# Optimization experiments

Hardware: AMD Instinct MI355X
Metric: run time of the kernel (lower is better)

Reference implementation:

```python
import jax, jax.numpy as jnp
import numpy as np
from jax import lax

DIM = 256
NUM_HEADS = 8
HEAD_DIM = DIM // NUM_HEADS          # 32
KEY_DIM = int(HEAD_DIM * 0.5)        # 16
SCALE = KEY_DIM ** -0.5
H_QKV = DIM + KEY_DIM * NUM_HEADS * 2  # 512
BN_EPS = 1e-3  # keras BatchNormalization default epsilon


def conv_bn(x, w, gamma, beta, mean, var, groups=1):
    # Conv2D (no bias) + BatchNorm (inference), activation=None
    y = lax.conv_general_dilated(
        x, w, window_strides=(1, 1), padding='SAME',
        dimension_numbers=('NHWC', 'HWIO', 'NHWC'),
        feature_group_count=groups)
    return gamma * (y - mean) * lax.rsqrt(var + BN_EPS) + beta


def setup_inputs() -> dict:
    key = jax.random.key(0)
    ks = jax.random.split(key, 4)
    B, Hs, Ws = 8, 32, 32
    inp = {
        'inputs': jax.random.normal(ks[0], (B, Hs, Ws, DIM), dtype=jnp.float32),
        # qkv: 1x1 conv dim -> h
        'qkv_w': jax.random.normal(ks[1], (1, 1, DIM, H_QKV), dtype=jnp.float32) * 0.05,
        'qkv_gamma': jnp.ones((H_QKV,), jnp.float32),
        'qkv_beta': jnp.zeros((H_QKV,), jnp.float32),
        'qkv_mean': jnp.zeros((H_QKV,), jnp.float32),
        'qkv_var': jnp.ones((H_QKV,), jnp.float32),
        # pe: 3x3 depthwise conv (groups=dim)
        'pe_w': jax.random.normal(ks[2], (3, 3, 1, DIM), dtype=jnp.float32) * 0.05,
        'pe_gamma': jnp.ones((DIM,), jnp.float32),
        'pe_beta': jnp.zeros((DIM,), jnp.float32),
        'pe_mean': jnp.zeros((DIM,), jnp.float32),
        'pe_var': jnp.ones((DIM,), jnp.float32),
        # proj: 1x1 conv dim -> dim
        'proj_w': jax.random.normal(ks[3], (1, 1, DIM, DIM), dtype=jnp.float32) * 0.05,
        'proj_gamma': jnp.ones((DIM,), jnp.float32),
        'proj_beta': jnp.zeros((DIM,), jnp.float32),
        'proj_mean': jnp.zeros((DIM,), jnp.float32),
        'proj_var': jnp.ones((DIM,), jnp.float32),
    }
    return inp


def reference(inputs, qkv_w, qkv_gamma, qkv_beta, qkv_mean, qkv_var,
              pe_w, pe_gamma, pe_beta, pe_mean, pe_var,
              proj_w, proj_gamma, proj_beta, proj_mean, proj_var):
    B, Hs, Ws, C = inputs.shape
    N = Hs * Ws
    x = conv_bn(inputs, qkv_w, qkv_gamma, qkv_beta, qkv_mean, qkv_var)  # [B,H,W,h]
    x = x.reshape(B, N, NUM_HEADS, 2 * KEY_DIM + HEAD_DIM)
    q = x[..., :KEY_DIM]                          # [B,N,nh,kd]
    k = x[..., KEY_DIM:2 * KEY_DIM]               # [B,N,nh,kd]
    v = x[..., 2 * KEY_DIM:]                      # [B,N,nh,hd]
    # attn = q^T @ k^T : [B,nh,N,N]
    attn = jnp.einsum('bnhk,bmhk->bhnm', q, k) * SCALE
    attn = jax.nn.softmax(attn, axis=-1)
    # x = v^T @ attn : [B,nh,hd,N]
    x = jnp.einsum('bnhd,bhnm->bhdm', v, attn)
    # faithful to source: transpose [0,2,1,3] -> [B,hd,nh,N], then reshape NHWC
    x = jnp.transpose(x, (0, 2, 1, 3)).reshape(B, Hs, Ws, C)
    pe = conv_bn(v.reshape(B, Hs, Ws, C), pe_w, pe_gamma, pe_beta, pe_mean, pe_var, groups=C)
    x = x + pe
    x = conv_bn(x, proj_w, proj_gamma, proj_beta, proj_mean, proj_var)
    return x
```

## Files before the change

### kernel.cpp

```cpp
#include <hip/hip_runtime.h>

typedef _Float16 h4 __attribute__((ext_vector_type(4)));
typedef _Float16 h8 __attribute__((ext_vector_type(8)));
typedef float    f4 __attribute__((ext_vector_type(4)));

#define QSCALE (0.25f * 1.44269504088896f)

__device__ __forceinline__ float ex2(float x){ return __builtin_amdgcn_exp2f(x); }

__global__ __launch_bounds__(256) void prep_k(
    const float* __restrict__ qkvw, const float* __restrict__ qg, const float* __restrict__ qb,
    const float* __restrict__ qm,   const float* __restrict__ qv,
    const float* __restrict__ pew,  const float* __restrict__ pg, const float* __restrict__ pb,
    const float* __restrict__ pm,   const float* __restrict__ pv,
    const float* __restrict__ prw,  const float* __restrict__ prg, const float* __restrict__ prb,
    const float* __restrict__ prm,  const float* __restrict__ prv,
    _Float16* __restrict__ Wqkv, float* __restrict__ bqkv,
    _Float16* __restrict__ Wproj, float* __restrict__ bproj,
    float* __restrict__ peW, float* __restrict__ peB)
{
  const int gid = blockIdx.x*256 + threadIdx.x;
  const int gsz = gridDim.x*256;
  for (int i = gid; i < 512*256; i += gsz){
    int o = i >> 8, c = i & 255;
    float s = qg[o] * rsqrtf(qv[o] + 1e-3f);
    Wqkv[i] = (_Float16)(qkvw[c*512 + o] * s);
  }
  for (int i = gid; i < 512; i += gsz){
    float s = qg[i] * rsqrtf(qv[i] + 1e-3f);
    bqkv[i] = qb[i] - qm[i]*s;
  }
  for (int i = gid; i < 256*256; i += gsz){
    int o = i >> 8, c = i & 255;
    float s = prg[o] * rsqrtf(prv[o] + 1e-3f);
    Wproj[i] = (_Float16)(prw[c*256 + o] * s);
  }
  for (int i = gid; i < 256; i += gsz){
    float s = prg[i] * rsqrtf(prv[i] + 1e-3f);
    bproj[i] = prb[i] - prm[i]*s;
  }
  for (int i = gid; i < 9*256; i += gsz){
    int c = i & 255;
    float s = pg[c] * rsqrtf(pv[c] + 1e-3f);
    peW[i] = pew[i] * s;
  }
  for (int i = gid; i < 256; i += gsz){
    float s = pg[i] * rsqrtf(pv[i] + 1e-3f);
    peB[i] = pb[i] - pm[i]*s;
  }
}

__global__ __launch_bounds__(256) void qkv_gemm_k(
    const float* __restrict__ X, const _Float16* __restrict__ Wqkv,
    const float* __restrict__ bias,
    _Float16* __restrict__ Qh, _Float16* __restrict__ Kh, _Float16* __restrict__ Vh)
{
  __shared__ __align__(16) _Float16 As[64*136];
  __shared__ __align__(16) _Float16 Bs[64*136];
  const int t = threadIdx.x, lane = t & 63, wv = t >> 6;
  const int l15 = lane & 15, q = lane >> 4;
  const int wr = wv & 1, wc = wv >> 1;
  const int m0 = blockIdx.x*64, n0 = blockIdx.y*64;
  float4 av[8]; uint4 bv[4];
  #pragma unroll
  for (int i = 0; i < 8; ++i){
    int idx = i*256 + t, row = idx >> 5, c4 = idx & 31;
    av[i] = *(const float4*)(X + (size_t)(m0+row)*256 + c4*4);
  }
  #pragma unroll
  for (int i = 0; i < 4; ++i){
    int idx = i*256 + t, row = idx >> 4, seg = idx & 15;
    bv[i] = *(const uint4*)(Wqkv + (size_t)(n0+row)*256 + seg*8);
  }
  f4 acc[2][2] = {};
  #pragma unroll
  for (int kc = 0; kc < 2; ++kc){
    #pragma unroll
    for (int i = 0; i < 8; ++i){
      int idx = i*256 + t, row = idx >> 5, c4 = idx & 31;
      h4 o; o[0]=(_Float16)av[i].x; o[1]=(_Float16)av[i].y;
            o[2]=(_Float16)av[i].z; o[3]=(_Float16)av[i].w;
      *(h4*)&As[row*136 + c4*4] = o;
    }
    #pragma unroll
    for (int i = 0; i < 4; ++i){
      int idx = i*256 + t, row = idx >> 4, seg = idx & 15;
      *(uint4*)&Bs[row*136 + seg*8] = bv[i];
    }
    __syncthreads();
    if (kc == 0){
      #pragma unroll
      for (int i = 0; i < 8; ++i){
        int idx = i*256 + t, row = idx >> 5, c4 = idx & 31;
        av[i] = *(const float4*)(X + (size_t)(m0+row)*256 + 128 + c4*4);
      }
      #pragma unroll
      for (int i = 0; i < 4; ++i){
        int idx = i*256 + t, row = idx >> 4, seg = idx & 15;
        bv[i] = *(const uint4*)(Wqkv + (size_t)(n0+row)*256 + 128 + seg*8);
      }
    }
    #pragma unroll
    for (int kk = 0; kk < 4; ++kk){
      h8 af[2], bf[2];
      #pragma unroll
      for (int mi = 0; mi < 2; ++mi)
        af[mi] = *(const h8*)&As[(wr*32 + mi*16 + l15)*136 + kk*32 + q*8];
      #pragma unroll
      for (int nj = 0; nj < 2; ++nj)
        bf[nj] = *(const h8*)&Bs[(wc*32 + nj*16 + l15)*136 + kk*32 + q*8];
      #pragma unroll
      for (int mi = 0; mi < 2; ++mi)
      #pragma unroll
      for (int nj = 0; nj < 2; ++nj)
        acc[mi][nj] = __builtin_amdgcn_mfma_f32_16x16x32_f16(af[mi], bf[nj], acc[mi][nj], 0,0,0);
    }
    __syncthreads();
  }
  #pragma unroll
  for (int mi = 0; mi < 2; ++mi)
  #pragma unroll
  for (int nj = 0; nj < 2; ++nj){
    const int og = n0 + wc*32 + nj*16 + l15;
    const int h = og >> 6, j = og & 63;
    const float bs = bias[og];
    #pragma unroll
    for (int r = 0; r < 4; ++r){
      const int mg = m0 + wr*32 + mi*16 + q*4 + r;
      const int b = mg >> 10, n = mg & 1023;
      const size_t bhn = (size_t)(b*8+h)*1024 + n;
      const float v = acc[mi][nj][r] + bs;
      if (j < 16)      Qh[bhn*16 + j]      = (_Float16)(v * QSCALE);
      else if (j < 32) Kh[bhn*16 + (j-16)] = (_Float16)v;
      else             Vh[bhn*32 + (j-32)] = (_Float16)v;
    }
  }
}

__global__ __launch_bounds__(256) void proj_gemm_k(
    const _Float16* __restrict__ A, const _Float16* __restrict__ Wproj,
    const float* __restrict__ bias, float* __restrict__ Out)
{
  __shared__ __align__(16) _Float16 As[64*136];
  __shared__ __align__(16) _Float16 Bs[64*136];
  const int t = threadIdx.x, lane = t & 63, wv = t >> 6;
  const int l15 = lane & 15, q = lane >> 4;
  const int wr = wv & 1, wc = wv >> 1;
  const int m0 = blockIdx.x*64, n0 = blockIdx.y*64;
  uint4 av[4], bv[4];
  #pragma unroll
  for (int i = 0; i < 4; ++i){
    int idx = i*256 + t, row = idx >> 4, seg = idx & 15;
    av[i] = *(const uint4*)(A     + (size_t)(m0+row)*256 + seg*8);
    bv[i] = *(const uint4*)(Wproj + (size_t)(n0+row)*256 + seg*8);
  }
  f4 acc[2][2] = {};
  #pragma unroll
  for (int kc = 0; kc < 2; ++kc){
    #pragma unroll
    for (int i = 0; i < 4; ++i){
      int idx = i*256 + t, row = idx >> 4, seg = idx & 15;
      *(uint4*)&As[row*136 + seg*8] = av[i];
      *(uint4*)&Bs[row*136 + seg*8] = bv[i];
    }
    __syncthreads();
    if (kc == 0){
      #pragma unroll
      for (int i = 0; i < 4; ++i){
        int idx = i*256 + t, row = idx >> 4, seg = idx & 15;
        av[i] = *(const uint4*)(A     + (size_t)(m0+row)*256 + 128 + seg*8);
        bv[i] = *(const uint4*)(Wproj + (size_t)(n0+row)*256 + 128 + seg*8);
      }
    }
    #pragma unroll
    for (int kk = 0; kk < 4; ++kk){
      h8 af[2], bf[2];
      #pragma unroll
      for (int mi = 0; mi < 2; ++mi)
        af[mi] = *(const h8*)&As[(wr*32 + mi*16 + l15)*136 + kk*32 + q*8];
      #pragma unroll
      for (int nj = 0; nj < 2; ++nj)
        bf[nj] = *(const h8*)&Bs[(wc*32 + nj*16 + l15)*136 + kk*32 + q*8];
      #pragma unroll
      for (int mi = 0; mi < 2; ++mi)
      #pragma unroll
      for (int nj = 0; nj < 2; ++nj)
        acc[mi][nj] = __builtin_amdgcn_mfma_f32_16x16x32_f16(af[mi], bf[nj], acc[mi][nj], 0,0,0);
    }
    __syncthreads();
  }
  #pragma unroll
  for (int mi = 0; mi < 2; ++mi)
  #pragma unroll
  for (int nj = 0; nj < 2; ++nj){
    const int og = n0 + wc*32 + nj*16 + l15;
    const float bs = bias[og];
    #pragma unroll
    for (int r = 0; r < 4; ++r){
      const int mg = m0 + wr*32 + mi*16 + q*4 + r;
      Out[(size_t)mg*256 + og] = acc[mi][nj][r] + bs;
    }
  }
}

__global__ __launch_bounds__(256) void pass1_k(
    const _Float16* __restrict__ Qh, const _Float16* __restrict__ Kh,
    const _Float16* __restrict__ Vh, _Float16* __restrict__ Vs)
{
  __shared__ __align__(16) _Float16 Ks[128*24];
  const int t = threadIdx.x, lane = t & 63, wv = t >> 6;
  const int l15 = lane & 15, q = lane >> 4;
  const int bh = blockIdx.x;
  const int n0 = blockIdx.y*128 + wv*32;
  const size_t qb = (size_t)bh*1024;
  const h4 af0 = *(const h4*)(Qh + (qb + n0 + l15)*16 + q*4);
  const h4 af1 = *(const h4*)(Qh + (qb + n0 + 16 + l15)*16 + q*4);
  const _Float16* kp = Kh + qb*16;
  const int row = t >> 1, seg = t & 1;
  uint4 kr = *(const uint4*)(kp + row*16 + seg*8);
  f4 sm0 = {0.f,0.f,0.f,0.f}, sm1 = {0.f,0.f,0.f,0.f};
  for (int c = 0; c < 8; ++c){
    *(uint4*)&Ks[row*24 + seg*8] = kr;
    __syncthreads();
    if (c < 7) kr = *(const uint4*)(kp + ((c+1)*128 + row)*16 + seg*8);
    #pragma unroll
    for (int sub = 0; sub < 8; ++sub){
      h4 bf = *(const h4*)&Ks[(sub*16 + l15)*24 + q*4];
      f4 z = {0.f,0.f,0.f,0.f};
      f4 d0 = __builtin_amdgcn_mfma_f32_16x16x16f16(af0, bf, z, 0,0,0);
      f4 d1 = __builtin_amdgcn_mfma_f32_16x16x16f16(af1, bf, z, 0,0,0);
      #pragma unroll
      for (int r = 0; r < 4; ++r){ sm0[r] += ex2(d0[r]); sm1[r] += ex2(d1[r]); }
    }
    __syncthreads();
  }
  #pragma unroll
  for (int st = 1; st < 16; st <<= 1){
    #pragma unroll
    for (int r = 0; r < 4; ++r){
      sm0[r] += __shfl_xor(sm0[r], st, 64);
      sm1[r] += __shfl_xor(sm1[r], st, 64);
    }
  }
  f4 cv0, cv1;
  #pragma unroll
  for (int r = 0; r < 4; ++r){ cv0[r] = 1.0f/sm0[r]; cv1[r] = 1.0f/sm1[r]; }
  #pragma unroll
  for (int half = 0; half < 2; ++half){
    const int dd = l15 + half*16;
    h4 o0, o1;
    #pragma unroll
    for (int r = 0; r < 4; ++r){
      o0[r] = (_Float16)((float)Vh[(qb + n0 + q*4 + r)*32 + dd] * cv0[r]);
      o1[r] = (_Float16)((float)Vh[(qb + n0 + 16 + q*4 + r)*32 + dd] * cv1[r]);
    }
    *(h4*)(Vs + ((size_t)bh*32 + dd)*1024 + n0 + q*4)      = o0;
    *(h4*)(Vs + ((size_t)bh*32 + dd)*1024 + n0 + 16 + q*4) = o1;
  }
}

__global__ __launch_bounds__(256) void pass2_k(
    const _Float16* __restrict__ Qh, const _Float16* __restrict__ Kh,
    const _Float16* __restrict__ Vs, _Float16* __restrict__ X1h)
{
  __shared__ __align__(16) char smem[16896];
  _Float16* Qs  = (_Float16*)smem;
  _Float16* Vss = (_Float16*)(smem + 6144);
  float*    Tt  = (float*)smem;
  const int t = threadIdx.x, lane = t & 63, wv = t >> 6;
  const int l15 = lane & 15, q = lane >> 4;
  const int bh = blockIdx.x;
  const int b  = bh >> 3, h = bh & 7;
  const int mb = blockIdx.y*128 + wv*32;
  const size_t qb = (size_t)bh*1024;
  const h4 kf0 = *(const h4*)(Kh + (qb + mb + l15)*16 + q*4);
  const h4 kf1 = *(const h4*)(Kh + (qb + mb + 16 + l15)*16 + q*4);
  const _Float16* qp = Qh + qb*16;
  const _Float16* vp = Vs + (size_t)bh*32*1024;
  const int row = t >> 1, seg = t & 1;
  const int vd = t >> 4, vseg = t & 15;
  uint4 qr = *(const uint4*)(qp + row*16 + seg*8);
  uint4 vr0 = *(const uint4*)(vp + (size_t)vd*1024      + vseg*8);
  uint4 vr1 = *(const uint4*)(vp + (size_t)(vd+16)*1024 + vseg*8);
  f4 a00={0.f,0.f,0.f,0.f}, a01={0.f,0.f,0.f,0.f};
  f4 a10={0.f,0.f,0.f,0.f}, a11={0.f,0.f,0.f,0.f};
  for (int c = 0; c < 8; ++c){
    *(uint4*)&Qs[row*24 + seg*8] = qr;
    *(uint4*)&Vss[vd*136      + vseg*8] = vr0;
    *(uint4*)&Vss[(vd+16)*136 + vseg*8] = vr1;
    __syncthreads();
    if (c < 7){
      const int nn = (c+1)*128;
      qr  = *(const uint4*)(qp + (nn + row)*16 + seg*8);
      vr0 = *(const uint4*)(vp + (size_t)vd*1024      + nn + vseg*8);
      vr1 = *(const uint4*)(vp + (size_t)(vd+16)*1024 + nn + vseg*8);
    }
    #pragma unroll
    for (int sub = 0; sub < 8; ++sub){
      h4 qf = *(const h4*)&Qs[(sub*16 + l15)*24 + q*4];
      h4 b0 = *(const h4*)&Vss[l15*136      + sub*16 + q*4];
      h4 b1 = *(const h4*)&Vss[(16+l15)*136 + sub*16 + q*4];
      f4 z = {0.f,0.f,0.f,0.f};
      f4 s0 = __builtin_amdgcn_mfma_f32_16x16x16f16(qf, kf0, z, 0,0,0);
      f4 s1 = __builtin_amdgcn_mfma_f32_16x16x16f16(qf, kf1, z, 0,0,0);
      h4 p0, p1;
      #pragma unroll
      for (int r = 0; r < 4; ++r){ p0[r] = (_Float16)ex2(s0[r]); p1[r] = (_Float16)ex2(s1[r]); }
      a00 = __builtin_amdgcn_mfma_f32_16x16x16f16(p0, b0, a00, 0,0,0);
      a01 = __builtin_amdgcn_mfma_f32_16x16x16f16(p0, b1, a01, 0,0,0);
      a10 = __builtin_amdgcn_mfma_f32_16x16x16f16(p1, b0, a10, 0,0,0);
      a11 = __builtin_amdgcn_mfma_f32_16x16x16f16(p1, b1, a11, 0,0,0);
    }
    __syncthreads();
  }
  float* tw = Tt + wv*(32*33);
  #pragma unroll
  for (int r = 0; r < 4; ++r){
    tw[(q*4 + r)*33      + l15]      = a00[r];
    tw[(q*4 + r)*33      + 16 + l15] = a01[r];
    tw[(16 + q*4 + r)*33 + l15]      = a10[r];
    tw[(16 + q*4 + r)*33 + 16 + l15] = a11[r];
  }
  __syncthreads();
  _Float16* xb = X1h + (size_t)b*262144 + (size_t)h*1024 + mb;
  const int mloc = lane & 31, dh = lane >> 5;
  #pragma unroll
  for (int r = 0; r < 16; ++r){
    const int d = r*2 + dh;
    xb[(size_t)d*8192 + mloc] = (_Float16)tw[mloc*33 + d];
  }
}

__global__ __launch_bounds__(256) void pe_add_k(
    const _Float16* __restrict__ Vh, const _Float16* __restrict__ X1h,
    const float* __restrict__ peW, const float* __restrict__ peB,
    _Float16* __restrict__ X2h)
{
  const int u = blockIdx.x*256 + threadIdx.x;
  const int c0 = (u & 31) * 8;
  const int tok = u >> 5;
  const int b = tok >> 10, n = tok & 1023;
  const int hs = n >> 5, ws = n & 31;
  const int h = c0 >> 5, d0 = c0 & 31;
  const size_t idx8 = (size_t)tok*256 + c0;
  float acc[8];
  {
    f4 b0v = *(const f4*)(peB + c0), b1v = *(const f4*)(peB + c0 + 4);
    #pragma unroll
    for (int j = 0; j < 4; ++j){ acc[j] = b0v[j]; acc[4+j] = b1v[j]; }
  }
  const _Float16* vb = Vh + (size_t)(b*8 + h)*32768 + d0;
  #pragma unroll
  for (int dy = 0; dy < 3; ++dy){
    const int y = hs + dy - 1;
    if ((unsigned)y < 32u){
      #pragma unroll
      for (int dx = 0; dx < 3; ++dx){
        const int x = ws + dx - 1;
        if ((unsigned)x < 32u){
          const int kk = dy*3 + dx;
          h8 vv = *(const h8*)(vb + (size_t)(y*32 + x)*32);
          f4 w0 = *(const f4*)(peW + kk*256 + c0);
          f4 w1 = *(const f4*)(peW + kk*256 + c0 + 4);
          #pragma unroll
          for (int j = 0; j < 4; ++j){
            acc[j]   += w0[j] * (float)vv[j];
            acc[4+j] += w1[j] * (float)vv[4+j];
          }
        }
      }
    }
  }
  h8 x1 = *(const h8*)(X1h + idx8);
  h8 o;
  #pragma unroll
  for (int j = 0; j < 8; ++j) o[j] = (_Float16)((float)x1[j] + acc[j]);
  *(h8*)(X2h + idx8) = o;
}

extern "C" void kernel_launch(void* const* d_in, const int* in_sizes, int n_in,
                              void* d_out, int out_size, void* d_ws, size_t ws_size,
                              hipStream_t stream)
{
  const float* X    = (const float*)d_in[0];
  const float* qkvw = (const float*)d_in[1];
  const float* qg   = (const float*)d_in[2];
  const float* qb   = (const float*)d_in[3];
  const float* qm   = (const float*)d_in[4];
  const float* qv   = (const float*)d_in[5];
  const float* pew  = (const float*)d_in[6];
  const float* pg   = (const float*)d_in[7];
  const float* pb   = (const float*)d_in[8];
  const float* pm   = (const float*)d_in[9];
  const float* pv   = (const float*)d_in[10];
  const float* prw  = (const float*)d_in[11];
  const float* prg  = (const float*)d_in[12];
  const float* prb  = (const float*)d_in[13];
  const float* prm  = (const float*)d_in[14];
  const float* prv  = (const float*)d_in[15];

  char* ws = (char*)d_ws;
  _Float16* X2h   = (_Float16*)(ws + 0);
  _Float16* Qh    = (_Float16*)(ws + 4194304);
  _Float16* Kh    = (_Float16*)(ws + 6291456);
  _Float16* Vh    = (_Float16*)(ws + 8388608);
  _Float16* Vs    = (_Float16*)(ws + 12582912);
  _Float16* X1h   = (_Float16*)(ws + 16777216);
  _Float16* Wqkv  = (_Float16*)(ws + 20971520);
  float*    bqkv  = (float*)   (ws + 21233664);
  _Float16* Wproj = (_Float16*)(ws + 21235712);
  float*    bproj = (float*)   (ws + 21366784);
  float*    peW   = (float*)   (ws + 21367808);
  float*    peB   = (float*)   (ws + 21377024);

  prep_k<<<64, 256, 0, stream>>>(qkvw, qg, qb, qm, qv, pew, pg, pb, pm, pv,
                                 prw, prg, prb, prm, prv,
                                 Wqkv, bqkv, Wproj, bproj, peW, peB);
  qkv_gemm_k<<<dim3(128, 8), 256, 0, stream>>>(X, Wqkv, bqkv, Qh, Kh, Vh);
  pass1_k<<<dim3(64, 8), 256, 0, stream>>>(Qh, Kh, Vh, Vs);
  pass2_k<<<dim3(64, 8), 256, 0, stream>>>(Qh, Kh, Vs, X1h);
  pe_add_k<<<1024, 256, 0, stream>>>(Vh, X1h, peW, peB, X2h);
  proj_gemm_k<<<dim3(128, 4), 256, 0, stream>>>(X2h, Wproj, bproj, (float*)d_out);
}
```

Measured before the change: 159.1 us.

## Fuse depthwise PE conv into attention pass2 and widen QKV GEMM tiles

Removes the separate pe_add kernel by computing the 3x3 depthwise positional-encoding conv inside pass2's epilogue. It maps each output element back to its source V channel and adds the result before writing X2h, so the X1h intermediate round trip and one launch go away. The QKV GEMM now loads the full K=256 A tile once into LDS and loops over four N sub-tiles per block, reusing the converted input across 256 output columns. The cost is fewer GEMM blocks (256 instead of 1024), a larger LDS footprint, and scalar, uncoalesced V gathers in the fused epilogue.

```diff
diff --git a/kernel.cpp b/kernel.cpp
--- a/kernel.cpp
+++ b/kernel.cpp
@@ -55,85 +55,75 @@
     const float* __restrict__ bias,
     _Float16* __restrict__ Qh, _Float16* __restrict__ Kh, _Float16* __restrict__ Vh)
 {
-  __shared__ __align__(16) _Float16 As[64*136];
-  __shared__ __align__(16) _Float16 Bs[64*136];
+  __shared__ __align__(16) _Float16 As[64*264];
+  __shared__ __align__(16) _Float16 Bs[64*264];
   const int t = threadIdx.x, lane = t & 63, wv = t >> 6;
   const int l15 = lane & 15, q = lane >> 4;
   const int wr = wv & 1, wc = wv >> 1;
-  const int m0 = blockIdx.x*64, n0 = blockIdx.y*64;
-  float4 av[8]; uint4 bv[4];
+  const int m0 = blockIdx.x*64, nbase = blockIdx.y*256;
+  #pragma unroll
+  for (int i = 0; i < 16; ++i){
+    int idx = i*256 + t, row = idx >> 6, c4 = idx & 63;
+    float4 v = *(const float4*)(X + (size_t)(m0+row)*256 + c4*4);
+    h4 o; o[0]=(_Float16)v.x; o[1]=(_Float16)v.y; o[2]=(_Float16)v.z; o[3]=(_Float16)v.w;
+    *(h4*)&As[row*264 + c4*4] = o;
+  }
+  uint4 bv[8];
   #pragma unroll
   for (int i = 0; i < 8; ++i){
-    int idx = i*256 + t, row = idx >> 5, c4 = idx & 31;
-    av[i] = *(const float4*)(X + (size_t)(m0+row)*256 + c4*4);
-  }
-  #pragma unroll
-  for (int i = 0; i < 4; ++i){
-    int idx = i*256 + t, row = idx >> 4, seg = idx & 15;
-    bv[i] = *(const uint4*)(Wqkv + (size_t)(n0+row)*256 + seg*8);
-  }
-  f4 acc[2][2] = {};
-  #pragma unroll
-  for (int kc = 0; kc < 2; ++kc){
+    int idx = i*256 + t, row = idx >> 5, seg = idx & 31;
+    bv[i] = *(const uint4*)(Wqkv + (size_t)(nbase+row)*256 + seg*8);
+  }
+  for (int nt = 0; nt < 4; ++nt){
+    const int n0 = nbase + nt*64;
     #pragma unroll
     for (int i = 0; i < 8; ++i){
-      int idx = i*256 + t, row = idx >> 5, c4 = idx & 31;
-      h4 o; o[0]=(_Float16)av[i].x; o[1]=(_Float16)av[i].y;
-            o[2]=(_Float16)av[i].z; o[3]=(_Float16)av[i].w;
-      *(h4*)&As[row*136 + c4*4] = o;
-    }
-    #pragma unroll
-    for (int i = 0; i < 4; ++i){
-      int idx = i*256 + t, row = idx >> 4, seg = idx & 15;
-      *(uint4*)&Bs[row*136 + seg*8] = bv[i];
-    }
-    __syncthreads();
-    if (kc == 0){
+      int idx = i*256 + t, row = idx >> 5, seg = idx & 31;
+      *(uint4*)&Bs[row*264 + seg*8] = bv[i];
+    }
+    __syncthreads();
+    if (nt < 3){
       #pragma unroll
       for (int i = 0; i < 8; ++i){
-        int idx = i*256 + t, row = idx >> 5, c4 = idx & 31;
-        av[i] = *(const float4*)(X + (size_t)(m0+row)*256 + 128 + c4*4);
+        int idx = i*256 + t, row = idx >> 5, seg = idx & 31;
+        bv[i] = *(const uint4*)(Wqkv + (size_t)(n0 + 64 + row)*256 + seg*8);
       }
-      #pragma unroll
-      for (int i = 0; i < 4; ++i){
-        int idx = i*256 + t, row = idx >> 4, seg = idx & 15;
-        bv[i] = *(const uint4*)(Wqkv + (size_t)(n0+row)*256 + 128 + seg*8);
-      }
-    }
-    #pragma unroll
-    for (int kk = 0; kk < 4; ++kk){
+    }
+    f4 acc[2][2] = {};
+    #pragma unroll
+    for (int kk = 0; kk < 8; ++kk){
       h8 af[2], bf[2];
       #pragma unroll
       for (int mi = 0; mi < 2; ++mi)
-        af[mi] = *(const h8*)&As[(wr*32 + mi*16 + l15)*136 + kk*32 + q*8];
+        af[mi] = *(const h8*)&As[(wr*32 + mi*16 + l15)*264 + kk*32 + q*8];
       #pragma unroll
       for (int nj = 0; nj < 2; ++nj)
-        bf[nj] = *(const h8*)&Bs[(wc*32 + nj*16 + l15)*136 + kk*32 + q*8];
+        bf[nj] = *(const h8*)&Bs[(wc*32 + nj*16 + l15)*264 + kk*32 + q*8];
       #pragma unroll
       for (int mi = 0; mi < 2; ++mi)
       #pragma unroll
       for (int nj = 0; nj < 2; ++nj)
         acc[mi][nj] = __builtin_amdgcn_mfma_f32_16x16x32_f16(af[mi], bf[nj], acc[mi][nj], 0,0,0);
     }
-    __syncthreads();
-  }
-  #pragma unroll
-  for (int mi = 0; mi < 2; ++mi)
-  #pragma unroll
-  for (int nj = 0; nj < 2; ++nj){
-    const int og = n0 + wc*32 + nj*16 + l15;
-    const int h = og >> 6, j = og & 63;
-    const float bs = bias[og];
-    #pragma unroll
-    for (int r = 0; r < 4; ++r){
-      const int mg = m0 + wr*32 + mi*16 + q*4 + r;
-      const int b = mg >> 10, n = mg & 1023;
-      const size_t bhn = (size_t)(b*8+h)*1024 + n;
-      const float v = acc[mi][nj][r] + bs;
-      if (j < 16)      Qh[bhn*16 + j]      = (_Float16)(v * QSCALE);
-      else if (j < 32) Kh[bhn*16 + (j-16)] = (_Float16)v;
-      else             Vh[bhn*32 + (j-32)] = (_Float16)v;
-    }
+    #pragma unroll
+    for (int mi = 0; mi < 2; ++mi)
+    #pragma unroll
+    for (int nj = 0; nj < 2; ++nj){
+      const int og = n0 + wc*32 + nj*16 + l15;
+      const int h = og >> 6, j = og & 63;
+      const float bs = bias[og];
+      #pragma unroll
+      for (int r = 0; r < 4; ++r){
+        const int mg = m0 + wr*32 + mi*16 + q*4 + r;
+        const int b = mg >> 10, n = mg & 1023;
+        const size_t bhn = (size_t)(b*8+h)*1024 + n;
+        const float v = acc[mi][nj][r] + bs;
+        if (j < 16)      Qh[bhn*16 + j]      = (_Float16)(v * QSCALE);
+        else if (j < 32) Kh[bhn*16 + (j-16)] = (_Float16)v;
+        else             Vh[bhn*32 + (j-32)] = (_Float16)v;
+      }
+    }
+    __syncthreads();
   }
 }
 
@@ -261,7 +251,9 @@
 
 __global__ __launch_bounds__(256) void pass2_k(
     const _Float16* __restrict__ Qh, const _Float16* __restrict__ Kh,
-    const _Float16* __restrict__ Vs, _Float16* __restrict__ X1h)
+    const _Float16* __restrict__ Vs, const _Float16* __restrict__ Vh,
+    const float* __restrict__ peW, const float* __restrict__ peB,
+    _Float16* __restrict__ X2h)
 {
   __shared__ __align__(16) char smem[16896];
   _Float16* Qs  = (_Float16*)smem;
@@ -271,7 +263,8 @@
   const int l15 = lane & 15, q = lane >> 4;
   const int bh = blockIdx.x;
   const int b  = bh >> 3, h = bh & 7;
-  const int mb = blockIdx.y*128 + wv*32;
+  const int y  = blockIdx.y;
+  const int mb = y*128 + wv*32;
   const size_t qb = (size_t)bh*1024;
   const h4 kf0 = *(const h4*)(Kh + (qb + mb + l15)*16 + q*4);
   const h4 kf1 = *(const h4*)(Kh + (qb + mb + 16 + l15)*16 + q*4);
@@ -322,60 +315,34 @@
     tw[(16 + q*4 + r)*33 + 16 + l15] = a11[r];
   }
   __syncthreads();
-  _Float16* xb = X1h + (size_t)b*262144 + (size_t)h*1024 + mb;
   const int mloc = lane & 31, dh = lane >> 5;
+  const int wsx = h*4 + (y >> 1);
+  const int c_out = (y & 1)*128 + wv*32 + mloc;
+  const int h2 = c_out >> 5;
+  const _Float16* vb2 = Vh + (size_t)(b*8 + h2)*32768 + mloc;
+  float w9[9];
+  #pragma unroll
+  for (int kk2 = 0; kk2 < 9; ++kk2) w9[kk2] = peW[kk2*256 + c_out];
+  const float pbv = peB[c_out];
+  _Float16* xb = X2h + (size_t)b*262144 + (size_t)h*1024 + mb;
   #pragma unroll
   for (int r = 0; r < 16; ++r){
     const int d = r*2 + dh;
-    xb[(size_t)d*8192 + mloc] = (_Float16)tw[mloc*33 + d];
-  }
-}
-
-__global__ __launch_bounds__(256) void pe_add_k(
-    const _Float16* __restrict__ Vh, const _Float16* __restrict__ X1h,
-    const float* __restrict__ peW, const float* __restrict__ peB,
-    _Float16* __restrict__ X2h)
-{
-  const int u = blockIdx.x*256 + threadIdx.x;
-  const int c0 = (u & 31) * 8;
-  const int tok = u >> 5;
-  const int b = tok >> 10, n = tok & 1023;
-  const int hs = n >> 5, ws = n & 31;
-  const int h = c0 >> 5, d0 = c0 & 31;
-  const size_t idx8 = (size_t)tok*256 + c0;
-  float acc[8];
-  {
-    f4 b0v = *(const f4*)(peB + c0), b1v = *(const f4*)(peB + c0 + 4);
-    #pragma unroll
-    for (int j = 0; j < 4; ++j){ acc[j] = b0v[j]; acc[4+j] = b1v[j]; }
-  }
-  const _Float16* vb = Vh + (size_t)(b*8 + h)*32768 + d0;
-  #pragma unroll
-  for (int dy = 0; dy < 3; ++dy){
-    const int y = hs + dy - 1;
-    if ((unsigned)y < 32u){
-      #pragma unroll
-      for (int dx = 0; dx < 3; ++dx){
-        const int x = ws + dx - 1;
-        if ((unsigned)x < 32u){
-          const int kk = dy*3 + dx;
-          h8 vv = *(const h8*)(vb + (size_t)(y*32 + x)*32);
-          f4 w0 = *(const f4*)(peW + kk*256 + c0);
-          f4 w1 = *(const f4*)(peW + kk*256 + c0 + 4);
-          #pragma unroll
-          for (int j = 0; j < 4; ++j){
-            acc[j]   += w0[j] * (float)vv[j];
-            acc[4+j] += w1[j] * (float)vv[4+j];
-          }
+    float pe = pbv;
+    #pragma unroll
+    for (int dy = 0; dy < 3; ++dy){
+      const int yy = d + dy - 1;
+      if ((unsigned)yy < 32u){
+        #pragma unroll
+        for (int dx = 0; dx < 3; ++dx){
+          const int xx = wsx + dx - 1;
+          if ((unsigned)xx < 32u)
+            pe += w9[dy*3+dx] * (float)vb2[(size_t)(yy*32 + xx)*32];
         }
       }
     }
-  }
-  h8 x1 = *(const h8*)(X1h + idx8);
-  h8 o;
-  #pragma unroll
-  for (int j = 0; j < 8; ++j) o[j] = (_Float16)((float)x1[j] + acc[j]);
-  *(h8*)(X2h + idx8) = o;
+    xb[(size_t)d*8192 + mloc] = (_Float16)(tw[mloc*33 + d] + pe);
+  }
 }
 
 extern "C" void kernel_launch(void* const* d_in, const int* in_sizes, int n_in,
@@ -405,20 +372,18 @@
   _Float16* Kh    = (_Float16*)(ws + 6291456);
   _Float16* Vh    = (_Float16*)(ws + 8388608);
   _Float16* Vs    = (_Float16*)(ws + 12582912);
-  _Float16* X1h   = (_Float16*)(ws + 16777216);
-  _Float16* Wqkv  = (_Float16*)(ws + 20971520);
-  float*    bqkv  = (float*)   (ws + 21233664);
-  _Float16* Wproj = (_Float16*)(ws + 21235712);
-  float*    bproj = (float*)   (ws + 21366784);
-  float*    peW   = (float*)   (ws + 21367808);
-  float*    peB   = (float*)   (ws + 21377024);
+  _Float16* Wqkv  = (_Float16*)(ws + 16777216);
+  float*    bqkv  = (float*)   (ws + 17039360);
+  _Float16* Wproj = (_Float16*)(ws + 17041408);
+  float*    bproj = (float*)   (ws + 17172480);
+  float*    peW   = (float*)   (ws + 17173504);
+  float*    peB   = (float*)   (ws + 17182720);
 
   prep_k<<<64, 256, 0, stream>>>(qkvw, qg, qb, qm, qv, pew, pg, pb, pm, pv,
                                  prw, prg, prb, prm, prv,
                                  Wqkv, bqkv, Wproj, bproj, peW, peB);
-  qkv_gemm_k<<<dim3(128, 8), 256, 0, stream>>>(X, Wqkv, bqkv, Qh, Kh, Vh);
+  qkv_gemm_k<<<dim3(128, 2), 256, 0, stream>>>(X, Wqkv, bqkv, Qh, Kh, Vh);
   pass1_k<<<dim3(64, 8), 256, 0, stream>>>(Qh, Kh, Vh, Vs);
-  pass2_k<<<dim3(64, 8), 256, 0, stream>>>(Qh, Kh, Vs, X1h);
-  pe_add_k<<<1024, 256, 0, stream>>>(Vh, X1h, peW, peB, X2h);
+  pass2_k<<<dim3(64, 8), 256, 0, stream>>>(Qh, Kh, Vs, Vh, peW, peB, X2h);
   proj_gemm_k<<<dim3(128, 4), 256, 0, stream>>>(X2h, Wproj, bproj, (float*)d_out);
 }
```

Result: slower. 176.2 us (+10.8%).
